# Optimization experiments

Hardware: AMD Instinct MI355X
Metric: run time of the kernel (lower is better)

## Reference

```python
import jax, jax.numpy as jnp
import numpy as np

N_NODES = 50000
N_EDGES = 640000
NFEAT = 128
NHID = 128
BN_EPS = 1e-5
GIN_EPS = 0.0  # GINConv default eps


def setup_inputs() -> dict:
    key = jax.random.key(0)
    ks = jax.random.split(key, 8)
    x = jax.random.normal(ks[0], (N_NODES, NFEAT), dtype=jnp.float32)
    edge_index = jax.random.randint(ks[1], (2, N_EDGES), 0, N_NODES, dtype=jnp.int64)
    # xavier-uniform linears, zero bias (per weights_init); BN gamma=1, beta=0
    def xavier(k, fan_in, fan_out):
        a = float(np.sqrt(6.0 / (fan_in + fan_out)))
        return jax.random.uniform(k, (fan_in, fan_out), dtype=jnp.float32, minval=-a, maxval=a)
    W1 = xavier(ks[2], NFEAT, NHID)
    b1 = jnp.zeros((NHID,), dtype=jnp.float32)
    gamma = jnp.ones((NHID,), dtype=jnp.float32)
    beta = jnp.zeros((NHID,), dtype=jnp.float32)
    W2 = xavier(ks[3], NHID, NHID)
    b2 = jnp.zeros((NHID,), dtype=jnp.float32)
    return {"x": x, "edge_index": edge_index, "W1": W1, "b1": b1,
            "gamma": gamma, "beta": beta, "W2": W2, "b2": b2}


def reference(x, edge_index, W1, b1, gamma, beta, W2, b2):
    src, dst = edge_index[0], edge_index[1]
    # sparse neighbor sum-aggregation: agg[i] = sum_{(src->dst=i)} x[src]
    agg = jax.ops.segment_sum(x[src], dst, num_segments=x.shape[0])
    h = (1.0 + GIN_EPS) * x + agg
    # MLP: Linear -> ReLU -> BatchNorm1d (training-mode batch stats) -> Linear
    h = jax.nn.relu(h @ W1 + b1)
    mean = jnp.mean(h, axis=0)
    var = jnp.mean(jnp.square(h - mean), axis=0)  # biased var, as torch BN uses
    h = (h - mean) * jax.lax.rsqrt(var + BN_EPS) * gamma + beta
    return h @ W2 + b2
```

## Files before the change

kernel.cpp:

```cpp
#include <hip/hip_runtime.h>
#include <hip/hip_fp16.h>

#define NNODES 50000
#define NEDGES 640000
#define NF 128
#define XB 3125
#define BINS 196
#define BINCAP 4096
#define P1AB 313
#define EPB 2048

typedef __attribute__((ext_vector_type(8))) _Float16 f16x8;
typedef __attribute__((ext_vector_type(4))) float f32x4;

__global__ __launch_bounds__(256) void k_prep(const float* __restrict__ x,
                                              const int* __restrict__ ei,
                                              unsigned short* __restrict__ xh,
                                              int* __restrict__ cnt,
                                              float* __restrict__ stats) {
  __shared__ int lcnt[BINS];
  const int bid = blockIdx.x, t = threadIdx.x;
  if (bid < XB) {
    int i = bid * 256 + t;
    const float4 a = ((const float4*)x)[2 * i];
    const float4 b = ((const float4*)x)[2 * i + 1];
    __half2 h0 = __float22half2_rn(make_float2(a.x, a.y));
    __half2 h1 = __float22half2_rn(make_float2(a.z, a.w));
    __half2 h2 = __float22half2_rn(make_float2(b.x, b.y));
    __half2 h3 = __float22half2_rn(make_float2(b.z, b.w));
    uint4 v;
    v.x = *(unsigned*)&h0; v.y = *(unsigned*)&h1;
    v.z = *(unsigned*)&h2; v.w = *(unsigned*)&h3;
    ((uint4*)xh)[i] = v;
    if (bid == 0) { stats[t] = 0.f; stats[256 + t] = 0.f; }
  } else {
    const int blk = bid - XB;
    const int e0 = blk * EPB;
    const bool full = (e0 + EPB <= NEDGES);
    if (t < BINS) lcnt[t] = 0;
    __syncthreads();
    const int4 d0 = *(const int4*)(ei + NEDGES + e0 + 4 * t);
    atomicAdd(&lcnt[d0.x >> 8], 1);
    atomicAdd(&lcnt[d0.y >> 8], 1);
    atomicAdd(&lcnt[d0.z >> 8], 1);
    atomicAdd(&lcnt[d0.w >> 8], 1);
    if (full) {
      const int4 d1 = *(const int4*)(ei + NEDGES + e0 + 1024 + 4 * t);
      atomicAdd(&lcnt[d1.x >> 8], 1);
      atomicAdd(&lcnt[d1.y >> 8], 1);
      atomicAdd(&lcnt[d1.z >> 8], 1);
      atomicAdd(&lcnt[d1.w >> 8], 1);
    }
    __syncthreads();
    if (t < BINS) cnt[blk * BINS + t] = lcnt[t];
  }
}

__global__ __launch_bounds__(512) void k_p1b(const int* __restrict__ cnt,
                                             int* __restrict__ base,
                                             int* __restrict__ gtot) {
  __shared__ int s[512];
  const int t = threadIdx.x, b = blockIdx.x;
  const int v = (t < P1AB) ? cnt[t * BINS + b] : 0;
  s[t] = v;
  __syncthreads();
  for (int d = 1; d < 512; d <<= 1) {
    int u = (t >= d) ? s[t - d] : 0;
    __syncthreads();
    s[t] += u;
    __syncthreads();
  }
  if (t < P1AB) base[t * BINS + b] = s[t] - v;
  if (t == 511) gtot[b] = s[511];
}

__global__ __launch_bounds__(256) void k_p1c(const int* __restrict__ ei,
                                             const int* __restrict__ base,
                                             unsigned* __restrict__ binbuf) {
  __shared__ int lcur[BINS];
  const int t = threadIdx.x, blk = blockIdx.x;
  const int e0 = blk * EPB;
  const bool full = (e0 + EPB <= NEDGES);
  if (t < BINS) lcur[t] = base[blk * BINS + t];
  __syncthreads();
  const int4 s0 = *(const int4*)(ei + e0 + 4 * t);
  const int4 d0 = *(const int4*)(ei + NEDGES + e0 + 4 * t);
#define SCAT(ss, dd)                                                             \
  {                                                                              \
    int bin = (dd) >> 8;                                                         \
    int pos = atomicAdd(&lcur[bin], 1);                                          \
    if (pos < BINCAP)                                                            \
      binbuf[bin * BINCAP + pos] = ((unsigned)((dd) & 255) << 16) | (unsigned)(ss); \
  }
  SCAT(s0.x, d0.x); SCAT(s0.y, d0.y); SCAT(s0.z, d0.z); SCAT(s0.w, d0.w);
  if (full) {
    const int4 s1 = *(const int4*)(ei + e0 + 1024 + 4 * t);
    const int4 d1 = *(const int4*)(ei + NEDGES + e0 + 1024 + 4 * t);
    SCAT(s1.x, d1.x); SCAT(s1.y, d1.y); SCAT(s1.z, d1.z); SCAT(s1.w, d1.w);
  }
#undef SCAT
}

__global__ __launch_bounds__(256) void k_p2(const unsigned* __restrict__ binbuf,
                                            const int* __restrict__ gtot,
                                            int* __restrict__ begdeg,
                                            unsigned short* __restrict__ slot) {
  __shared__ int cnt2[256], pst[256];
  __shared__ unsigned short stg[BINCAP];
  const int t = threadIdx.x;
  const int b = blockIdx.x;
  const int base = b * BINCAP;
  const int nb = min(gtot[b], BINCAP);
  unsigned pk[16];
#pragma unroll
  for (int ci = 0; ci < 16; ++ci) {
    int i = (ci << 8) + t;
    pk[ci] = (i < nb) ? binbuf[base + i] : 0xFFFFFFFFu;
  }
  cnt2[t] = 0;
  __syncthreads();
#pragma unroll
  for (int ci = 0; ci < 16; ++ci)
    if (pk[ci] != 0xFFFFFFFFu) atomicAdd(&cnt2[(int)(pk[ci] >> 16)], 1);
  __syncthreads();
  pst[t] = cnt2[t];
  __syncthreads();
  for (int d = 1; d < 256; d <<= 1) {
    int u = (t >= d) ? pst[t - d] : 0;
    __syncthreads();
    pst[t] += u;
    __syncthreads();
  }
  pst[t] -= cnt2[t];
  int node = (b << 8) + t;
  if (node < NNODES)
    begdeg[node] = ((base + pst[t]) << 8) | min(cnt2[t], 255);
  cnt2[t] = 0;
  __syncthreads();
#pragma unroll
  for (int ci = 0; ci < 16; ++ci)
    if (pk[ci] != 0xFFFFFFFFu) {
      int dl = (int)(pk[ci] >> 16);
      int pos = atomicAdd(&cnt2[dl], 1);
      stg[pst[dl] + pos] = (unsigned short)(pk[ci] & 0xffffu);
    }
  __syncthreads();
  for (int i = t; i < nb; i += 256) slot[base + i] = stg[i];
}

__device__ inline void add8h(float* a, uint4 v) {
  const __half2* p = (const __half2*)&v;
#pragma unroll
  for (int q = 0; q < 4; ++q) {
    float2 f = __half22float2(p[q]);
    a[2 * q] += f.x;
    a[2 * q + 1] += f.y;
  }
}

__global__ __launch_bounds__(256) void k_gather(const unsigned short* __restrict__ xh,
                                                const int* __restrict__ begdeg,
                                                const unsigned short* __restrict__ slot,
                                                _Float16* __restrict__ h) {
  const int t = threadIdx.x;
  const int wv = t >> 6, l = t & 63;
  const int node = blockIdx.x * 4 + wv;
  if (node >= NNODES) return;
  const int cg_ = (l & 15) << 3;
  const int e = l >> 4;
  const int bd = begdeg[node];
  const int beg = bd >> 8;
  const int end = beg + (bd & 255);
  float a[8] = {0.f, 0.f, 0.f, 0.f, 0.f, 0.f, 0.f, 0.f};
  float b[8] = {0.f, 0.f, 0.f, 0.f, 0.f, 0.f, 0.f, 0.f};
  int j = beg + e;
  for (; j + 4 < end; j += 8) {
    const uint4 v0 = *(const uint4*)(xh + (size_t)slot[j] * NF + cg_);
    const uint4 v1 = *(const uint4*)(xh + (size_t)slot[j + 4] * NF + cg_);
    add8h(a, v0);
    add8h(b, v1);
  }
  if (j < end) {
    const uint4 v0 = *(const uint4*)(xh + (size_t)slot[j] * NF + cg_);
    add8h(a, v0);
  }
#pragma unroll
  for (int q = 0; q < 8; ++q) a[q] += b[q];
#pragma unroll
  for (int q = 0; q < 8; ++q) {
    a[q] += __shfl_xor(a[q], 16);
    a[q] += __shfl_xor(a[q], 32);
  }
  if (e == 0) {
    const uint4 sv = *(const uint4*)(xh + (size_t)node * NF + cg_);
    add8h(a, sv);
    f16x8 o;
#pragma unroll
    for (int q = 0; q < 8; ++q) o[q] = (_Float16)a[q];
    *(f16x8*)(h + (size_t)node * NF + cg_) = o;
  }
}

template <int MODE>
__global__ __launch_bounds__(256, 2) void k_gemm(const _Float16* __restrict__ A,
                                                 const float* __restrict__ W,
                                                 const float* __restrict__ bias,
                                                 const float* __restrict__ gamma,
                                                 const float* __restrict__ beta,
                                                 float* __restrict__ stats,
                                                 _Float16* __restrict__ outh,
                                                 float* __restrict__ outf) {
  __shared__ _Float16 wl[32768];
  __shared__ float red[2][4][128];
  __shared__ float scs[128], shs[128], b2sh[128];

  const int t = threadIdx.x;
  const int wv = t >> 6;
  const int l = t & 63;
  const int wrow0 = blockIdx.x * 128 + wv * 16;

  f16x8 areg[2][4];
#pragma unroll
  for (int m = 0; m < 2; ++m) {
    const int arow = wrow0 + m * 64 + (l & 15);
    const bool okA = arow < NNODES;
#pragma unroll
    for (int ks = 0; ks < 4; ++ks) {
      if (okA) {
        areg[m][ks] = *(const f16x8*)(A + (size_t)arow * NF + ks * 32 + ((l >> 4) << 3));
      } else {
        areg[m][ks] = (f16x8){};
      }
    }
  }

  if (MODE == 1) {
    if (t < 128) {
      const float inv = 1.0f / (float)NNODES;
      float mean = stats[t] * inv;
      float var = fmaxf(stats[128 + t] * inv - mean * mean, 0.f);
      float sc = gamma[t] * rsqrtf(var + 1e-5f);
      scs[t] = sc;
      shs[t] = beta[t] - mean * sc;
    }
    __syncthreads();
  }

#pragma unroll
  for (int oct = 0; oct < 8; ++oct) {
    int f8 = oct * 256 + t;
    int ks = f8 >> 9, cf = (f8 >> 6) & 7, lane = f8 & 63;
    int k0 = ks * 32 + ((lane >> 4) << 3);
    int n = cf * 16 + (lane & 15);
    f16x8 hi, lo;
#pragma unroll
    for (int j = 0; j < 8; ++j) {
      float w = W[(k0 + j) * NF + n];
      if (MODE == 1) w *= scs[k0 + j];
      _Float16 h_ = (_Float16)w;
      hi[j] = h_;
      lo[j] = (_Float16)(w - (float)h_);
    }
    *(f16x8*)(wl + f8 * 8) = hi;
    *(f16x8*)(wl + 16384 + f8 * 8) = lo;
  }

  if (MODE == 1) {
    const int col = t & 127, half = t >> 7;
    float s = 0.f;
    for (int k = half * 64; k < half * 64 + 64; ++k) s += shs[k] * W[k * NF + col];
    red[0][half][col] = s;
  }
  __syncthreads();
  if (MODE == 1) {
    if (t < 128) b2sh[t] = bias[t] + red[0][0][t] + red[0][1][t];
    __syncthreads();
  }

  f32x4 acc[2][8];
#pragma unroll
  for (int m = 0; m < 2; ++m)
#pragma unroll
    for (int cf = 0; cf < 8; ++cf) acc[m][cf] = (f32x4){0.f, 0.f, 0.f, 0.f};

#pragma unroll
  for (int ks = 0; ks < 4; ++ks) {
#pragma unroll
    for (int cf = 0; cf < 8; ++cf) {
      const int fo = (((ks * 8 + cf) << 6) + l) << 3;
      f16x8 bh = *(const f16x8*)(wl + fo);
      f16x8 bl = *(const f16x8*)(wl + 16384 + fo);
#pragma unroll
      for (int m = 0; m < 2; ++m) {
        acc[m][cf] = __builtin_amdgcn_mfma_f32_16x16x32_f16(areg[m][ks], bh, acc[m][cf], 0, 0, 0);
        acc[m][cf] = __builtin_amdgcn_mfma_f32_16x16x32_f16(areg[m][ks], bl, acc[m][cf], 0, 0, 0);
      }
    }
  }

  const int col16 = l & 15;
  const int rg = l >> 4;
  float bl_[8];
#pragma unroll
  for (int cf = 0; cf < 8; ++cf)
    bl_[cf] = (MODE == 0) ? bias[cf * 16 + col16] : b2sh[cf * 16 + col16];

  if (MODE == 0) {
    float cs[8], cq[8];
#pragma unroll
    for (int cf = 0; cf < 8; ++cf) { cs[cf] = 0.f; cq[cf] = 0.f; }
#pragma unroll
    for (int m = 0; m < 2; ++m)
#pragma unroll
      for (int cf = 0; cf < 8; ++cf) {
#pragma unroll
        for (int r = 0; r < 4; ++r) {
          int row = wrow0 + m * 64 + rg * 4 + r;
          if (row < NNODES) {
            float v = fmaxf(acc[m][cf][r] + bl_[cf], 0.f);
            outh[(size_t)row * NF + cf * 16 + col16] = (_Float16)v;
            cs[cf] += v;
            cq[cf] += v * v;
          }
        }
      }
#pragma unroll
    for (int cf = 0; cf < 8; ++cf) {
      cs[cf] += __shfl_xor(cs[cf], 16); cs[cf] += __shfl_xor(cs[cf], 32);
      cq[cf] += __shfl_xor(cq[cf], 16); cq[cf] += __shfl_xor(cq[cf], 32);
    }
    __syncthreads();
    if (l < 16) {
#pragma unroll
      for (int cf = 0; cf < 8; ++cf) {
        red[0][wv][cf * 16 + l] = cs[cf];
        red[1][wv][cf * 16 + l] = cq[cf];
      }
    }
    __syncthreads();
    if (t < 128) {
      float s = red[0][0][t] + red[0][1][t] + red[0][2][t] + red[0][3][t];
      float q = red[1][0][t] + red[1][1][t] + red[1][2][t] + red[1][3][t];
      unsafeAtomicAdd(stats + t, s);
      unsafeAtomicAdd(stats + 128 + t, q);
    }
  } else {
#pragma unroll
    for (int m = 0; m < 2; ++m)
#pragma unroll
      for (int cf = 0; cf < 8; ++cf) {
#pragma unroll
        for (int r = 0; r < 4; ++r) {
          int row = wrow0 + m * 64 + rg * 4 + r;
          if (row < NNODES)
            outf[(size_t)row * NF + cf * 16 + col16] = acc[m][cf][r] + bl_[cf];
        }
      }
  }
}

extern "C" void kernel_launch(void* const* d_in, const int* in_sizes, int n_in,
                              void* d_out, int out_size, void* d_ws, size_t ws_size,
                              hipStream_t stream) {
  const float* x     = (const float*)d_in[0];
  const int*   ei    = (const int*)d_in[1];
  const float* W1    = (const float*)d_in[2];
  const float* b1    = (const float*)d_in[3];
  const float* gamma = (const float*)d_in[4];
  const float* beta  = (const float*)d_in[5];
  const float* W2    = (const float*)d_in[6];
  const float* b2    = (const float*)d_in[7];
  float* out = (float*)d_out;

  _Float16* h = (_Float16*)d_out;

  float*          stats  = (float*)d_ws;
  int*            cnt    = (int*)(stats + 512);
  int*            basep  = cnt + 61376;
  int*            gtot   = basep + 61376;
  int*            begdeg = gtot + 256;
  unsigned*       binbuf = (unsigned*)(begdeg + 50176);
  unsigned short* slot   = (unsigned short*)(binbuf + BINS * BINCAP);
  unsigned short* xh     = slot + BINS * BINCAP;
  _Float16*       h1     = (_Float16*)(xh + (size_t)NNODES * NF);

  k_prep   <<<XB + P1AB, 256, 0, stream>>>(x, ei, xh, cnt, stats);
  k_p1b    <<<BINS, 512, 0, stream>>>(cnt, basep, gtot);
  k_p1c    <<<P1AB, 256, 0, stream>>>(ei, basep, binbuf);
  k_p2     <<<BINS, 256, 0, stream>>>(binbuf, gtot, begdeg, slot);
  k_gather <<<(NNODES + 3) / 4, 256, 0, stream>>>(xh, begdeg, slot, h);
  k_gemm<0><<<(NNODES + 127) / 128, 256, 0, stream>>>(h, W1, b1, nullptr, nullptr,
                                                      stats, h1, nullptr);
  k_gemm<1><<<(NNODES + 127) / 128, 256, 0, stream>>>(h1, W2, b2, gamma, beta,
                                                      stats, nullptr, out);
}
```

Measured before the change: 88.85 us.

## Apply W1 before aggregation, fuse ReLU/BN stats into gather, drop scan kernel

Uses linearity to compute x@W1 first, fused into the prep kernel alongside edge binning, so the gather sums projected rows and applies bias, ReLU and the BatchNorm statistic accumulation directly. This removes the separate first GEMM pass and the fp16 conversion pass over x. The separate per-bin prefix-scan kernel is replaced by a transposed count layout that k_p1c scans serially per bin and k_p2 reduces for bin totals. BN statistics are spread over 32 replicated accumulators to reduce atomic contention. The trade-off is an fp16 rounding of xW before summation and a serial scan loop in k_p1c whose length grows with block index.

```diff
diff --git a/kernel.cpp b/kernel.cpp
--- a/kernel.cpp
+++ b/kernel.cpp
@@ -4,40 +4,114 @@
 #define NNODES 50000
 #define NEDGES 640000
 #define NF 128
-#define XB 3125
+#define GB 391
+#define HB 313
 #define BINS 196
 #define BINCAP 4096
-#define P1AB 313
 #define EPB 2048
+#define BPAD 320
+#define NREP 32
 
 typedef __attribute__((ext_vector_type(8))) _Float16 f16x8;
 typedef __attribute__((ext_vector_type(4))) float f32x4;
 
-__global__ __launch_bounds__(256) void k_prep(const float* __restrict__ x,
-                                              const int* __restrict__ ei,
-                                              unsigned short* __restrict__ xh,
-                                              int* __restrict__ cnt,
-                                              float* __restrict__ stats) {
+__global__ __launch_bounds__(256, 2) void k_prep(const float* __restrict__ x,
+                                                 const float* __restrict__ W1,
+                                                 const int* __restrict__ ei,
+                                                 _Float16* __restrict__ xw,
+                                                 int* __restrict__ cntT,
+                                                 float* __restrict__ rep) {
+  __shared__ _Float16 wl[32768];
   __shared__ int lcnt[BINS];
   const int bid = blockIdx.x, t = threadIdx.x;
-  if (bid < XB) {
-    int i = bid * 256 + t;
-    const float4 a = ((const float4*)x)[2 * i];
-    const float4 b = ((const float4*)x)[2 * i + 1];
-    __half2 h0 = __float22half2_rn(make_float2(a.x, a.y));
-    __half2 h1 = __float22half2_rn(make_float2(a.z, a.w));
-    __half2 h2 = __float22half2_rn(make_float2(b.x, b.y));
-    __half2 h3 = __float22half2_rn(make_float2(b.z, b.w));
-    uint4 v;
-    v.x = *(unsigned*)&h0; v.y = *(unsigned*)&h1;
-    v.z = *(unsigned*)&h2; v.w = *(unsigned*)&h3;
-    ((uint4*)xh)[i] = v;
-    if (bid == 0) { stats[t] = 0.f; stats[256 + t] = 0.f; }
+
+  if (bid < GB) {
+    const int wv = t >> 6;
+    const int l = t & 63;
+    const int wrow0 = bid * 128 + wv * 16;
+
+    f16x8 areg[2][4];
+#pragma unroll
+    for (int m = 0; m < 2; ++m) {
+      const int arow = wrow0 + m * 64 + (l & 15);
+      const bool okA = arow < NNODES;
+#pragma unroll
+      for (int ks = 0; ks < 4; ++ks) {
+        if (okA) {
+          const float* p = x + (size_t)arow * NF + ks * 32 + ((l >> 4) << 3);
+          const float4 a0 = *(const float4*)(p);
+          const float4 a1 = *(const float4*)(p + 4);
+          f16x8 v;
+          v[0] = (_Float16)a0.x; v[1] = (_Float16)a0.y;
+          v[2] = (_Float16)a0.z; v[3] = (_Float16)a0.w;
+          v[4] = (_Float16)a1.x; v[5] = (_Float16)a1.y;
+          v[6] = (_Float16)a1.z; v[7] = (_Float16)a1.w;
+          areg[m][ks] = v;
+        } else {
+          areg[m][ks] = (f16x8){};
+        }
+      }
+    }
+
+#pragma unroll
+    for (int oct = 0; oct < 8; ++oct) {
+      int f8 = oct * 256 + t;
+      int ks = f8 >> 9, cf = (f8 >> 6) & 7, lane = f8 & 63;
+      int k0 = ks * 32 + ((lane >> 4) << 3);
+      int n = cf * 16 + (lane & 15);
+      f16x8 hi, lo;
+#pragma unroll
+      for (int j = 0; j < 8; ++j) {
+        float w = W1[(k0 + j) * NF + n];
+        _Float16 h_ = (_Float16)w;
+        hi[j] = h_;
+        lo[j] = (_Float16)(w - (float)h_);
+      }
+      *(f16x8*)(wl + f8 * 8) = hi;
+      *(f16x8*)(wl + 16384 + f8 * 8) = lo;
+    }
+    __syncthreads();
+
+    f32x4 acc[2][8];
+#pragma unroll
+    for (int m = 0; m < 2; ++m)
+#pragma unroll
+      for (int cf = 0; cf < 8; ++cf) acc[m][cf] = (f32x4){0.f, 0.f, 0.f, 0.f};
+
+#pragma unroll
+    for (int ks = 0; ks < 4; ++ks) {
+#pragma unroll
+      for (int cf = 0; cf < 8; ++cf) {
+        const int fo = (((ks * 8 + cf) << 6) + l) << 3;
+        f16x8 bh = *(const f16x8*)(wl + fo);
+        f16x8 bl = *(const f16x8*)(wl + 16384 + fo);
+#pragma unroll
+        for (int m = 0; m < 2; ++m) {
+          acc[m][cf] = __builtin_amdgcn_mfma_f32_16x16x32_f16(areg[m][ks], bh, acc[m][cf], 0, 0, 0);
+          acc[m][cf] = __builtin_amdgcn_mfma_f32_16x16x32_f16(areg[m][ks], bl, acc[m][cf], 0, 0, 0);
+        }
+      }
+    }
+
+    const int col16 = l & 15;
+    const int rg = l >> 4;
+#pragma unroll
+    for (int m = 0; m < 2; ++m)
+#pragma unroll
+      for (int cf = 0; cf < 8; ++cf) {
+#pragma unroll
+        for (int r = 0; r < 4; ++r) {
+          int row = wrow0 + m * 64 + rg * 4 + r;
+          if (row < NNODES)
+            xw[(size_t)row * NF + cf * 16 + col16] = (_Float16)acc[m][cf][r];
+        }
+      }
   } else {
-    const int blk = bid - XB;
+    const int blk = bid - GB;
     const int e0 = blk * EPB;
     const bool full = (e0 + EPB <= NEDGES);
     if (t < BINS) lcnt[t] = 0;
+    if (blk < NREP) rep[blk * 256 + t] = 0.f;
     __syncthreads();
     const int4 d0 = *(const int4*)(ei + NEDGES + e0 + 4 * t);
     atomicAdd(&lcnt[d0.x >> 8], 1);
@@ -52,36 +126,23 @@
       atomicAdd(&lcnt[d1.w >> 8], 1);
     }
     __syncthreads();
-    if (t < BINS) cnt[blk * BINS + t] = lcnt[t];
-  }
-}
-
-__global__ __launch_bounds__(512) void k_p1b(const int* __restrict__ cnt,
-                                             int* __restrict__ base,
-                                             int* __restrict__ gtot) {
-  __shared__ int s[512];
-  const int t = threadIdx.x, b = blockIdx.x;
-  const int v = (t < P1AB) ? cnt[t * BINS + b] : 0;
-  s[t] = v;
-  __syncthreads();
-  for (int d = 1; d < 512; d <<= 1) {
-    int u = (t >= d) ? s[t - d] : 0;
-    __syncthreads();
-    s[t] += u;
-    __syncthreads();
-  }
-  if (t < P1AB) base[t * BINS + b] = s[t] - v;
-  if (t == 511) gtot[b] = s[511];
+    if (t < BINS) cntT[t * BPAD + blk] = lcnt[t];
+  }
 }
 
 __global__ __launch_bounds__(256) void k_p1c(const int* __restrict__ ei,
-                                             const int* __restrict__ base,
+                                             const int* __restrict__ cntT,
                                              unsigned* __restrict__ binbuf) {
   __shared__ int lcur[BINS];
   const int t = threadIdx.x, blk = blockIdx.x;
   const int e0 = blk * EPB;
   const bool full = (e0 + EPB <= NEDGES);
-  if (t < BINS) lcur[t] = base[blk * BINS + t];
+  if (t < BINS) {
+    int s = 0;
+    const int* row = cntT + t * BPAD;
+    for (int b2 = 0; b2 < blk; ++b2) s += row[b2];
+    lcur[t] = s;
+  }
   __syncthreads();
   const int4 s0 = *(const int4*)(ei + e0 + 4 * t);
   const int4 d0 = *(const int4*)(ei + NEDGES + e0 + 4 * t);
@@ -102,15 +163,30 @@
 }
 
 __global__ __launch_bounds__(256) void k_p2(const unsigned* __restrict__ binbuf,
-                                            const int* __restrict__ gtot,
+                                            const int* __restrict__ cntT,
                                             int* __restrict__ begdeg,
                                             unsigned short* __restrict__ slot) {
   __shared__ int cnt2[256], pst[256];
   __shared__ unsigned short stg[BINCAP];
+  __shared__ int nb_sh;
   const int t = threadIdx.x;
   const int b = blockIdx.x;
   const int base = b * BINCAP;
-  const int nb = min(gtot[b], BINCAP);
+
+  {
+    int v = (t < HB) ? cntT[b * BPAD + t] : 0;
+    if (t + 256 < HB) v += cntT[b * BPAD + t + 256];
+    pst[t] = v;
+    __syncthreads();
+    for (int d = 128; d > 0; d >>= 1) {
+      if (t < d) pst[t] += pst[t + d];
+      __syncthreads();
+    }
+    if (t == 0) nb_sh = min(pst[0], BINCAP);
+    __syncthreads();
+  }
+  const int nb = nb_sh;
+
   unsigned pk[16];
 #pragma unroll
   for (int ci = 0; ci < 16; ++ci) {
@@ -158,30 +234,33 @@
   }
 }
 
-__global__ __launch_bounds__(256) void k_gather(const unsigned short* __restrict__ xh,
+__global__ __launch_bounds__(256) void k_gather(const _Float16* __restrict__ xw,
+                                                const float* __restrict__ b1,
                                                 const int* __restrict__ begdeg,
                                                 const unsigned short* __restrict__ slot,
-                                                _Float16* __restrict__ h) {
+                                                _Float16* __restrict__ h1,
+                                                float* __restrict__ rep) {
+  __shared__ float sarr[4][128], sarr2[4][128];
   const int t = threadIdx.x;
   const int wv = t >> 6, l = t & 63;
   const int node = blockIdx.x * 4 + wv;
-  if (node >= NNODES) return;
   const int cg_ = (l & 15) << 3;
   const int e = l >> 4;
   const int bd = begdeg[node];
   const int beg = bd >> 8;
   const int end = beg + (bd & 255);
+  const unsigned short* xwu = (const unsigned short*)xw;
   float a[8] = {0.f, 0.f, 0.f, 0.f, 0.f, 0.f, 0.f, 0.f};
   float b[8] = {0.f, 0.f, 0.f, 0.f, 0.f, 0.f, 0.f, 0.f};
   int j = beg + e;
   for (; j + 4 < end; j += 8) {
-    const uint4 v0 = *(const uint4*)(xh + (size_t)slot[j] * NF + cg_);
-    const uint4 v1 = *(const uint4*)(xh + (size_t)slot[j + 4] * NF + cg_);
+    const uint4 v0 = *(const uint4*)(xwu + (size_t)slot[j] * NF + cg_);
+    const uint4 v1 = *(const uint4*)(xwu + (size_t)slot[j + 4] * NF + cg_);
     add8h(a, v0);
     add8h(b, v1);
   }
   if (j < end) {
-    const uint4 v0 = *(const uint4*)(xh + (size_t)slot[j] * NF + cg_);
+    const uint4 v0 = *(const uint4*)(xwu + (size_t)slot[j] * NF + cg_);
     add8h(a, v0);
   }
 #pragma unroll
@@ -192,26 +271,45 @@
     a[q] += __shfl_xor(a[q], 32);
   }
   if (e == 0) {
-    const uint4 sv = *(const uint4*)(xh + (size_t)node * NF + cg_);
+    const uint4 sv = *(const uint4*)(xwu + (size_t)node * NF + cg_);
     add8h(a, sv);
+    const float4 bb0 = *(const float4*)(b1 + cg_);
+    const float4 bb1 = *(const float4*)(b1 + cg_ + 4);
+    a[0] += bb0.x; a[1] += bb0.y; a[2] += bb0.z; a[3] += bb0.w;
+    a[4] += bb1.x; a[5] += bb1.y; a[6] += bb1.z; a[7] += bb1.w;
     f16x8 o;
 #pragma unroll
-    for (int q = 0; q < 8; ++q) o[q] = (_Float16)a[q];
-    *(f16x8*)(h + (size_t)node * NF + cg_) = o;
-  }
-}
-
-template <int MODE>
-__global__ __launch_bounds__(256, 2) void k_gemm(const _Float16* __restrict__ A,
-                                                 const float* __restrict__ W,
-                                                 const float* __restrict__ bias,
-                                                 const float* __restrict__ gamma,
-                                                 const float* __restrict__ beta,
-                                                 float* __restrict__ stats,
-                                                 _Float16* __restrict__ outh,
-                                                 float* __restrict__ outf) {
+    for (int q = 0; q < 8; ++q) {
+      float v = fmaxf(a[q], 0.f);
+      a[q] = v;
+      o[q] = (_Float16)v;
+    }
+    *(f16x8*)(h1 + (size_t)node * NF + cg_) = o;
+#pragma unroll
+    for (int q = 0; q < 8; ++q) {
+      sarr[wv][cg_ + q] = a[q];
+      sarr2[wv][cg_ + q] = a[q] * a[q];
+    }
+  }
+  __syncthreads();
+  if (t < 128) {
+    float s = sarr[0][t] + sarr[1][t] + sarr[2][t] + sarr[3][t];
+    float q = sarr2[0][t] + sarr2[1][t] + sarr2[2][t] + sarr2[3][t];
+    float* r = rep + (blockIdx.x & (NREP - 1)) * 256;
+    unsafeAtomicAdd(r + t, s);
+    unsafeAtomicAdd(r + 128 + t, q);
+  }
+}
+
+__global__ __launch_bounds__(256, 2) void k_gemm2(const _Float16* __restrict__ A,
+                                                  const float* __restrict__ W,
+                                                  const float* __restrict__ bias,
+                                                  const float* __restrict__ gamma,
+                                                  const float* __restrict__ beta,
+                                                  const float* __restrict__ rep,
+                                                  float* __restrict__ outf) {
   __shared__ _Float16 wl[32768];
-  __shared__ float red[2][4][128];
+  __shared__ float red[2][128];
   __shared__ float scs[128], shs[128], b2sh[128];
 
   const int t = threadIdx.x;
@@ -234,17 +332,21 @@
     }
   }
 
-  if (MODE == 1) {
-    if (t < 128) {
-      const float inv = 1.0f / (float)NNODES;
-      float mean = stats[t] * inv;
-      float var = fmaxf(stats[128 + t] * inv - mean * mean, 0.f);
-      float sc = gamma[t] * rsqrtf(var + 1e-5f);
-      scs[t] = sc;
-      shs[t] = beta[t] - mean * sc;
-    }
-    __syncthreads();
-  }
+  if (t < 128) {
+    float s = 0.f, q = 0.f;
+#pragma unroll
+    for (int r = 0; r < NREP; ++r) {
+      s += rep[r * 256 + t];
+      q += rep[r * 256 + 128 + t];
+    }
+    const float inv = 1.0f / (float)NNODES;
+    float mean = s * inv;
+    float var = fmaxf(q * inv - mean * mean, 0.f);
+    float sc = gamma[t] * rsqrtf(var + 1e-5f);
+    scs[t] = sc;
+    shs[t] = beta[t] - mean * sc;
+  }
+  __syncthreads();
 
 #pragma unroll
   for (int oct = 0; oct < 8; ++oct) {
@@ -255,8 +357,7 @@
     f16x8 hi, lo;
 #pragma unroll
     for (int j = 0; j < 8; ++j) {
-      float w = W[(k0 + j) * NF + n];
-      if (MODE == 1) w *= scs[k0 + j];
+      float w = W[(k0 + j) * NF + n] * scs[k0 + j];
       _Float16 h_ = (_Float16)w;
       hi[j] = h_;
       lo[j] = (_Float16)(w - (float)h_);
@@ -265,17 +366,15 @@
     *(f16x8*)(wl + 16384 + f8 * 8) = lo;
   }
 
-  if (MODE == 1) {
+  {
     const int col = t & 127, half = t >> 7;
     float s = 0.f;
     for (int k = half * 64; k < half * 64 + 64; ++k) s += shs[k] * W[k * NF + col];
-    red[0][half][col] = s;
-  }
-  __syncthreads();
-  if (MODE == 1) {
-    if (t < 128) b2sh[t] = bias[t] + red[0][0][t] + red[0][1][t];
-    __syncthreads();
-  }
+    red[half][col] = s;
+  }
+  __syncthreads();
+  if (t < 128) b2sh[t] = bias[t] + red[0][t] + red[1][t];
+  __syncthreads();
 
   f32x4 acc[2][8];
 #pragma unroll
@@ -300,63 +399,17 @@
 
   const int col16 = l & 15;
   const int rg = l >> 4;
-  float bl_[8];
-#pragma unroll
-  for (int cf = 0; cf < 8; ++cf)
-    bl_[cf] = (MODE == 0) ? bias[cf * 16 + col16] : b2sh[cf * 16 + col16];
-
-  if (MODE == 0) {
-    float cs[8], cq[8];
-#pragma unroll
-    for (int cf = 0; cf < 8; ++cf) { cs[cf] = 0.f; cq[cf] = 0.f; }
-#pragma unroll
-    for (int m = 0; m < 2; ++m)
-#pragma unroll
-      for (int cf = 0; cf < 8; ++cf) {
-#pragma unroll
-        for (int r = 0; r < 4; ++r) {
-          int row = wrow0 + m * 64 + rg * 4 + r;
-          if (row < NNODES) {
-            float v = fmaxf(acc[m][cf][r] + bl_[cf], 0.f);
-            outh[(size_t)row * NF + cf * 16 + col16] = (_Float16)v;
-            cs[cf] += v;
-            cq[cf] += v * v;
-          }
-        }
-      }
+#pragma unroll
+  for (int m = 0; m < 2; ++m)
 #pragma unroll
     for (int cf = 0; cf < 8; ++cf) {
-      cs[cf] += __shfl_xor(cs[cf], 16); cs[cf] += __shfl_xor(cs[cf], 32);
-      cq[cf] += __shfl_xor(cq[cf], 16); cq[cf] += __shfl_xor(cq[cf], 32);
-    }
-    __syncthreads();
-    if (l < 16) {
-#pragma unroll
-      for (int cf = 0; cf < 8; ++cf) {
-        red[0][wv][cf * 16 + l] = cs[cf];
-        red[1][wv][cf * 16 + l] = cq[cf];
-      }
-    }
-    __syncthreads();
-    if (t < 128) {
-      float s = red[0][0][t] + red[0][1][t] + red[0][2][t] + red[0][3][t];
-      float q = red[1][0][t] + red[1][1][t] + red[1][2][t] + red[1][3][t];
-      unsafeAtomicAdd(stats + t, s);
-      unsafeAtomicAdd(stats + 128 + t, q);
-    }
-  } else {
-#pragma unroll
-    for (int m = 0; m < 2; ++m)
-#pragma unroll
-      for (int cf = 0; cf < 8; ++cf) {
-#pragma unroll
-        for (int r = 0; r < 4; ++r) {
-          int row = wrow0 + m * 64 + rg * 4 + r;
-          if (row < NNODES)
-            outf[(size_t)row * NF + cf * 16 + col16] = acc[m][cf][r] + bl_[cf];
-        }
-      }
-  }
+#pragma unroll
+      for (int r = 0; r < 4; ++r) {
+        int row = wrow0 + m * 64 + rg * 4 + r;
+        if (row < NNODES)
+          outf[(size_t)row * NF + cf * 16 + col16] = acc[m][cf][r] + b2sh[cf * 16 + col16];
+      }
+    }
 }
 
 extern "C" void kernel_launch(void* const* d_in, const int* in_sizes, int n_in,
@@ -372,25 +425,18 @@
   const float* b2    = (const float*)d_in[7];
   float* out = (float*)d_out;
 
-  _Float16* h = (_Float16*)d_out;
-
-  float*          stats  = (float*)d_ws;
-  int*            cnt    = (int*)(stats + 512);
-  int*            basep  = cnt + 61376;
-  int*            gtot   = basep + 61376;
-  int*            begdeg = gtot + 256;
+  _Float16* xw = (_Float16*)d_out;
+
+  float*          rep    = (float*)d_ws;
+  int*            cntT   = (int*)(rep + NREP * 256);
+  int*            begdeg = cntT + BINS * BPAD;
   unsigned*       binbuf = (unsigned*)(begdeg + 50176);
   unsigned short* slot   = (unsigned short*)(binbuf + BINS * BINCAP);
-  unsigned short* xh     = slot + BINS * BINCAP;
-  _Float16*       h1     = (_Float16*)(xh + (size_t)NNODES * NF);
-
-  k_prep   <<<XB + P1AB, 256, 0, stream>>>(x, ei, xh, cnt, stats);
-  k_p1b    <<<BINS, 512, 0, stream>>>(cnt, basep, gtot);
-  k_p1c    <<<P1AB, 256, 0, stream>>>(ei, basep, binbuf);
-  k_p2     <<<BINS, 256, 0, stream>>>(binbuf, gtot, begdeg, slot);
-  k_gather <<<(NNODES + 3) / 4, 256, 0, stream>>>(xh, begdeg, slot, h);
-  k_gemm<0><<<(NNODES + 127) / 128, 256, 0, stream>>>(h, W1, b1, nullptr, nullptr,
-                                                      stats, h1, nullptr);
-  k_gemm<1><<<(NNODES + 127) / 128, 256, 0, stream>>>(h1, W2, b2, gamma, beta,
-                                                      stats, nullptr, out);
-}
+  _Float16*       h1     = (_Float16*)(slot + BINS * BINCAP);
+
+  k_prep  <<<GB + HB, 256, 0, stream>>>(x, W1, ei, xw, cntT, rep);
+  k_p1c   <<<HB, 256, 0, stream>>>(ei, cntT, binbuf);
+  k_p2    <<<BINS, 256, 0, stream>>>(binbuf, cntT, begdeg, slot);
+  k_gather<<<NNODES / 4, 256, 0, stream>>>(xw, b1, begdeg, slot, h1, rep);
+  k_gemm2 <<<(NNODES + 127) / 128, 256, 0, stream>>>(h1, W2, b2, gamma, beta, rep, out);
+}
```

New measurement: 96.38 us. 1.08x slower.

## Drop separate scan kernel by transposing bin counts and summing prefixes inline

Applied to the files above, without the earlier changes.

Removes the k_p1b exclusive-scan launch. Per-block bin counts are now stored transposed with padding, so each bin's counts are contiguous. k_p1c computes each block's prefix offset with a serial loop over earlier blocks, and k_p2 computes each bin's total with a shared-memory reduction. This saves one kernel launch and its dependency gap, but adds redundant serial work in k_p1c of up to about 312 loads per thread in late blocks.

```diff
diff --git a/kernel.cpp b/kernel.cpp
--- a/kernel.cpp
+++ b/kernel.cpp
@@ -7,8 +7,9 @@
 #define XB 3125
 #define BINS 196
 #define BINCAP 4096
-#define P1AB 313
+#define HB 313
 #define EPB 2048
+#define BPAD 320
 
 typedef __attribute__((ext_vector_type(8))) _Float16 f16x8;
 typedef __attribute__((ext_vector_type(4))) float f32x4;
@@ -16,7 +17,7 @@
 __global__ __launch_bounds__(256) void k_prep(const float* __restrict__ x,
                                               const int* __restrict__ ei,
                                               unsigned short* __restrict__ xh,
-                                              int* __restrict__ cnt,
+                                              int* __restrict__ cntT,
                                               float* __restrict__ stats) {
   __shared__ int lcnt[BINS];
   const int bid = blockIdx.x, t = threadIdx.x;
@@ -52,36 +53,23 @@
       atomicAdd(&lcnt[d1.w >> 8], 1);
     }
     __syncthreads();
-    if (t < BINS) cnt[blk * BINS + t] = lcnt[t];
-  }
-}
-
-__global__ __launch_bounds__(512) void k_p1b(const int* __restrict__ cnt,
-                                             int* __restrict__ base,
-                                             int* __restrict__ gtot) {
-  __shared__ int s[512];
-  const int t = threadIdx.x, b = blockIdx.x;
-  const int v = (t < P1AB) ? cnt[t * BINS + b] : 0;
-  s[t] = v;
-  __syncthreads();
-  for (int d = 1; d < 512; d <<= 1) {
-    int u = (t >= d) ? s[t - d] : 0;
-    __syncthreads();
-    s[t] += u;
-    __syncthreads();
-  }
-  if (t < P1AB) base[t * BINS + b] = s[t] - v;
-  if (t == 511) gtot[b] = s[511];
+    if (t < BINS) cntT[t * BPAD + blk] = lcnt[t];
+  }
 }
 
 __global__ __launch_bounds__(256) void k_p1c(const int* __restrict__ ei,
-                                             const int* __restrict__ base,
+                                             const int* __restrict__ cntT,
                                              unsigned* __restrict__ binbuf) {
   __shared__ int lcur[BINS];
   const int t = threadIdx.x, blk = blockIdx.x;
   const int e0 = blk * EPB;
   const bool full = (e0 + EPB <= NEDGES);
-  if (t < BINS) lcur[t] = base[blk * BINS + t];
+  if (t < BINS) {
+    int s = 0;
+    const int* row = cntT + t * BPAD;
+    for (int b2 = 0; b2 < blk; ++b2) s += row[b2];
+    lcur[t] = s;
+  }
   __syncthreads();
   const int4 s0 = *(const int4*)(ei + e0 + 4 * t);
   const int4 d0 = *(const int4*)(ei + NEDGES + e0 + 4 * t);
@@ -102,15 +90,30 @@
 }
 
 __global__ __launch_bounds__(256) void k_p2(const unsigned* __restrict__ binbuf,
-                                            const int* __restrict__ gtot,
+                                            const int* __restrict__ cntT,
                                             int* __restrict__ begdeg,
                                             unsigned short* __restrict__ slot) {
   __shared__ int cnt2[256], pst[256];
   __shared__ unsigned short stg[BINCAP];
+  __shared__ int nb_sh;
   const int t = threadIdx.x;
   const int b = blockIdx.x;
   const int base = b * BINCAP;
-  const int nb = min(gtot[b], BINCAP);
+
+  {
+    int v = (t < HB) ? cntT[b * BPAD + t] : 0;
+    if (t + 256 < HB) v += cntT[b * BPAD + t + 256];
+    pst[t] = v;
+    __syncthreads();
+    for (int d = 128; d > 0; d >>= 1) {
+      if (t < d) pst[t] += pst[t + d];
+      __syncthreads();
+    }
+    if (t == 0) nb_sh = min(pst[0], BINCAP);
+    __syncthreads();
+  }
+  const int nb = nb_sh;
+
   unsigned pk[16];
 #pragma unroll
   for (int ci = 0; ci < 16; ++ci) {
@@ -375,19 +378,16 @@
   _Float16* h = (_Float16*)d_out;
 
   float*          stats  = (float*)d_ws;
-  int*            cnt    = (int*)(stats + 512);
-  int*            basep  = cnt + 61376;
-  int*            gtot   = basep + 61376;
-  int*            begdeg = gtot + 256;
+  int*            cntT   = (int*)(stats + 512);
+  int*            begdeg = cntT + 62976;
   unsigned*       binbuf = (unsigned*)(begdeg + 50176);
   unsigned short* slot   = (unsigned short*)(binbuf + BINS * BINCAP);
   unsigned short* xh     = slot + BINS * BINCAP;
   _Float16*       h1     = (_Float16*)(xh + (size_t)NNODES * NF);
 
-  k_prep   <<<XB + P1AB, 256, 0, stream>>>(x, ei, xh, cnt, stats);
-  k_p1b    <<<BINS, 512, 0, stream>>>(cnt, basep, gtot);
-  k_p1c    <<<P1AB, 256, 0, stream>>>(ei, basep, binbuf);
-  k_p2     <<<BINS, 256, 0, stream>>>(binbuf, gtot, begdeg, slot);
+  k_prep   <<<XB + HB, 256, 0, stream>>>(x, ei, xh, cntT, stats);
+  k_p1c    <<<HB, 256, 0, stream>>>(ei, cntT, binbuf);
+  k_p2     <<<BINS, 256, 0, stream>>>(binbuf, cntT, begdeg, slot);
   k_gather <<<(NNODES + 3) / 4, 256, 0, stream>>>(xh, begdeg, slot, h);
   k_gemm<0><<<(NNODES + 127) / 128, 256, 0, stream>>>(h, W1, b1, nullptr, nullptr,
                                                       stats, h1, nullptr);
```

New measurement: 106.5 us. 1.2x slower.
